# Optimization experiments

Hardware: AMD Instinct MI355X
Metric: run time of the kernel (lower is better)

## Reference

```python
import jax, jax.numpy as jnp
import numpy as np
import math


def _conv1x1(x, w, b):
    # x: [B,C,H,W], w: [O,C], b: [O] -> [B,O,H,W]
    return jnp.einsum('oc,bchw->bohw', w, x) + b[None, :, None, None]


def _attn_branch(x, f_w, f_b, g_w, g_b, h_w, h_b, gamma):
    B, C, H, W = x.shape
    N = H * W
    k_dim = C // 8
    f = _conv1x1(x, f_w, f_b).reshape(B, k_dim, N)  # [B,k,N]
    g = _conv1x1(x, g_w, g_b).reshape(B, k_dim, N)  # [B,k,N]
    # attention[b, n, m] = sum_k f[b,k,n] * g[b,k,m] / sqrt(k_dim)
    scores = jnp.einsum('bkn,bkm->bnm', f, g) / math.sqrt(k_dim)
    attn = jax.nn.softmax(scores, axis=2)  # softmax over last dim (dim=2)
    h = _conv1x1(x, h_w, h_b).reshape(B, C, N)  # [B,C,N]
    sa_map = jnp.einsum('bcn,bnm->bcm', h, attn).reshape(B, C, H, W)
    return gamma[0] * sa_map + x


def setup_inputs() -> dict:
    key = jax.random.key(0)
    ks = jax.random.split(key, 8)
    B, C, H, W = 4, 256, 64, 64
    kd = C // 8
    scale_in = 1.0 / math.sqrt(C)
    return {
        'x1': jax.random.normal(ks[0], (B, C, H, W), jnp.float32),
        'x2': jax.random.normal(ks[1], (B, C, H, W), jnp.float32),
        'f_w': jax.random.normal(ks[2], (kd, C), jnp.float32) * scale_in,
        'f_b': jnp.zeros((kd,), jnp.float32),
        'g_w': jax.random.normal(ks[3], (kd, C), jnp.float32) * scale_in,
        'g_b': jnp.zeros((kd,), jnp.float32),
        'h1_w': jax.random.normal(ks[4], (C, C), jnp.float32) * scale_in,
        'h1_b': jnp.zeros((C,), jnp.float32),
        'h2_w': jax.random.normal(ks[5], (C, C), jnp.float32) * scale_in,
        'h2_b': jnp.zeros((C,), jnp.float32),
        'gamma1': jax.random.normal(ks[6], (1,), jnp.float32),
        'gamma2': jax.random.normal(ks[7], (1,), jnp.float32),
    }


def reference(x1, x2, f_w, f_b, g_w, g_b, h1_w, h1_b, h2_w, h2_b, gamma1, gamma2):
    y1 = _attn_branch(x1, f_w, f_b, g_w, g_b, h1_w, h1_b, gamma1)
    y2 = _attn_branch(x2, f_w, f_b, g_w, g_b, h2_w, h2_b, gamma2)
    return (y1, y2)
```

## Files before the change

kernel.cpp:

```cpp
#include <hip/hip_runtime.h>
#include <hip/hip_bf16.h>
#include <math.h>

#define NDIM 4096
#define CDIM 256
#define KD   32
#define SCALE 0.17677669529663687f
#define SHIFT 8.0f

typedef __attribute__((ext_vector_type(8))) short short8;
typedef __attribute__((ext_vector_type(4))) float f32x4;
typedef unsigned short u16;
typedef unsigned int u32;

__device__ __forceinline__ u32 f2bf(float x) {
  union { float f; u32 u; } v; v.f = x;
  return (v.u + 0x7FFFu + ((v.u >> 16) & 1u)) >> 16;
}

__device__ __forceinline__ u32 pack_bf16x2(float a, float b) {
  __hip_bfloat162 h2 = __float22bfloat162_rn(make_float2(a, b));
  u32 r;
  __builtin_memcpy(&r, &h2, 4);
  return r;
}

#define MFMA16(a, b, c) __builtin_amdgcn_mfma_f32_16x16x32_bf16((a), (b), (c), 0, 0, 0)

__global__ void cast_all_kernel(const float* __restrict__ h1w,
                                const float* __restrict__ h2w,
                                const float* __restrict__ fw,
                                const float* __restrict__ gw,
                                u16* __restrict__ dst) {
  int i = blockIdx.x * 256 + threadIdx.x;
  float v;
  if (i < 65536) v = h1w[i];
  else if (i < 131072) v = h2w[i - 65536];
  else if (i < 139264) v = fw[i - 131072];
  else v = gw[i - 139264];
  dst[i] = (u16)f2bf(v);
}

__global__ __launch_bounds__(256) void transpose_cast_kernel(
    const float* __restrict__ x1, const float* __restrict__ x2,
    u16* __restrict__ xt) {
  __shared__ float ts[64][68];
  const int t = threadIdx.x;
  const int ntile = blockIdx.x * 64, Ctile = blockIdx.y * 64, z = blockIdx.z;
  const float* xb = ((z >> 2) ? x2 : x1) + (size_t)(z & 3) * CDIM * NDIM;
  u16* xtb = xt + (size_t)z * NDIM * CDIM;
  const int r = t >> 4, c4 = (t & 15) * 4;
#pragma unroll
  for (int i = 0; i < 4; i++) {
    float4 v = *(const float4*)&xb[(size_t)(Ctile + r + i * 16) * NDIM + ntile + c4];
    *(float4*)&ts[r + i * 16][c4] = v;
  }
  __syncthreads();
  const int n = t >> 2, Cg = (t & 3) * 16;
  u32 pk[8];
#pragma unroll
  for (int j = 0; j < 8; j++) {
    u32 lo = f2bf(ts[Cg + 2 * j][n]);
    u32 hi = f2bf(ts[Cg + 2 * j + 1][n]);
    pk[j] = lo | (hi << 16);
  }
  uint4* dst = (uint4*)&xtb[(size_t)(ntile + n) * CDIM + Ctile + Cg];
  dst[0] = make_uint4(pk[0], pk[1], pk[2], pk[3]);
  dst[1] = make_uint4(pk[4], pk[5], pk[6], pk[7]);
}

__global__ __launch_bounds__(256) void conv_fg_kernel(
    const u16* __restrict__ Wf, const float* __restrict__ fbias,
    const u16* __restrict__ Wg, const float* __restrict__ gbias,
    const u16* __restrict__ xt, u16* __restrict__ ftT, u16* __restrict__ gtT) {
  const int t = threadIdx.x, w = t >> 6, l = t & 63, li = l & 15, q = l >> 4;
  const int ntile = blockIdx.x * 64, bb = blockIdx.y;
  const u16* xtb = xt + (size_t)bb * NDIM * CDIM;
  f32x4 zero4 = {0.f, 0.f, 0.f, 0.f};
  f32x4 acc[2][2];
  for (int i = 0; i < 2; i++) for (int j = 0; j < 2; j++) acc[i][j] = zero4;
  const int nrow = ntile + w * 16 + li;

  for (int k0 = 0; k0 < CDIM; k0 += 32) {
    short8 bx = *(const short8*)&xtb[(size_t)nrow * CDIM + k0 + q * 8];
    short8 af0 = *(const short8*)&Wf[(size_t)(li) * CDIM + k0 + q * 8];
    short8 af1 = *(const short8*)&Wf[(size_t)(16 + li) * CDIM + k0 + q * 8];
    short8 ag0 = *(const short8*)&Wg[(size_t)(li) * CDIM + k0 + q * 8];
    short8 ag1 = *(const short8*)&Wg[(size_t)(16 + li) * CDIM + k0 + q * 8];
    acc[0][0] = MFMA16(af0, bx, acc[0][0]);
    acc[0][1] = MFMA16(af1, bx, acc[0][1]);
    acc[1][0] = MFMA16(ag0, bx, acc[1][0]);
    acc[1][1] = MFMA16(ag1, bx, acc[1][1]);
  }
  u16* outs[2] = {ftT + (size_t)bb * NDIM * KD, gtT + (size_t)bb * NDIM * KD};
  const float* biases[2] = {fbias, gbias};
#pragma unroll
  for (int fg = 0; fg < 2; fg++) {
#pragma unroll
    for (int os = 0; os < 2; os++) {
      float b0 = biases[fg][os * 16 + q * 4 + 0];
      float b1 = biases[fg][os * 16 + q * 4 + 1];
      float b2 = biases[fg][os * 16 + q * 4 + 2];
      float b3 = biases[fg][os * 16 + q * 4 + 3];
      u32 p0 = f2bf(acc[fg][os][0] + b0) | (f2bf(acc[fg][os][1] + b1) << 16);
      u32 p1 = f2bf(acc[fg][os][2] + b2) | (f2bf(acc[fg][os][3] + b3) << 16);
      *(uint2*)&outs[fg][(size_t)nrow * KD + os * 16 + q * 4] = make_uint2(p0, p1);
    }
  }
}

__global__ __launch_bounds__(256) void stats_kernel(
    const u16* __restrict__ ft, const u16* __restrict__ gt,
    float* __restrict__ L) {
  __shared__ float zred[32][64];
  const int t = threadIdx.x, w = t >> 6, l = t & 63, li = l & 15, q = l >> 4;
  const int n0 = blockIdx.x * 32;
  const int bb = blockIdx.z * 4 + blockIdx.y;
  const u16* ftb = ft + (size_t)bb * NDIM * KD;
  const u16* gtb = gt + (size_t)bb * NDIM * KD;
  f32x4 zero4 = {0.f, 0.f, 0.f, 0.f};

  short8 a0 = *(const short8*)&ftb[(size_t)(n0 + li) * KD + q * 8];
  short8 a1 = *(const short8*)&ftb[(size_t)(n0 + 16 + li) * KD + q * 8];
  f32x4 z0 = zero4, z1 = zero4;

#pragma unroll 2
  for (int it = 0; it < 64; it++) {
    int m = (it * 4 + w) * 16;
    short8 bf = *(const short8*)&gtb[(size_t)(m + li) * KD + q * 8];
    f32x4 S0 = MFMA16(a0, bf, zero4);
    f32x4 S1 = MFMA16(a1, bf, zero4);
#pragma unroll
    for (int reg = 0; reg < 4; reg++) {
      z0[reg] += __expf(S0[reg] * SCALE - SHIFT);
      z1[reg] += __expf(S1[reg] * SCALE - SHIFT);
    }
  }
#pragma unroll
  for (int reg = 0; reg < 4; reg++) {
    zred[q * 4 + reg][w * 16 + li] = z0[reg];
    zred[16 + q * 4 + reg][w * 16 + li] = z1[reg];
  }
  __syncthreads();
  const int r = t >> 3, i8 = t & 7;
  float4 s1 = *(const float4*)&zred[r][i8 * 8];
  float4 s2 = *(const float4*)&zred[r][i8 * 8 + 4];
  float sum = s1.x + s1.y + s1.z + s1.w + s2.x + s2.y + s2.z + s2.w;
  sum += __shfl_xor(sum, 1, 8);
  sum += __shfl_xor(sum, 2, 8);
  sum += __shfl_xor(sum, 4, 8);
  if (i8 == 0) L[(size_t)bb * NDIM + n0 + r] = SHIFT + __logf(sum);
}

__global__ __launch_bounds__(256) void conv_h_kernel(
    const u16* __restrict__ Wall, const float* __restrict__ b1,
    const float* __restrict__ b2, const u16* __restrict__ xt,
    const float* __restrict__ L, u16* __restrict__ outH) {
  const int t = threadIdx.x, w = t >> 6, l = t & 63, li = l & 15, q = l >> 4;
  const int ntile = blockIdx.x * 64;
  const int o0 = blockIdx.y * 64 + w * 16;
  const int bb = blockIdx.z, branch = bb >> 2;
  const u16* W = Wall + (size_t)branch * CDIM * CDIM;
  const float* bias = branch ? b2 : b1;
  const u16* xtb = xt + (size_t)bb * NDIM * CDIM;
  const float* Lb = L + (size_t)bb * NDIM;
  u16* ob = outH + (size_t)bb * CDIM * NDIM;
  f32x4 zero4 = {0.f, 0.f, 0.f, 0.f};
  f32x4 acc[4];
  for (int i = 0; i < 4; i++) acc[i] = zero4;

  for (int k0 = 0; k0 < CDIM; k0 += 32) {
    short8 a = *(const short8*)&W[(size_t)(o0 + li) * CDIM + k0 + q * 8];
#pragma unroll
    for (int ns = 0; ns < 4; ns++) {
      short8 bf = *(const short8*)&xtb[(size_t)(ntile + ns * 16 + li) * CDIM + k0 + q * 8];
      acc[ns] = MFMA16(a, bf, acc[ns]);
    }
  }
  float bv[4];
#pragma unroll
  for (int reg = 0; reg < 4; reg++) bv[reg] = bias[o0 + q * 4 + reg];
#pragma unroll
  for (int ns = 0; ns < 4; ns++) {
    int n = ntile + ns * 16 + li;
    float ex = __expf(-Lb[n]);
#pragma unroll
    for (int reg = 0; reg < 4; reg++) {
      int c = o0 + q * 4 + reg;
      ob[(size_t)c * NDIM + n] = (u16)f2bf((acc[ns][reg] + bv[reg]) * ex);
    }
  }
}

__global__ __launch_bounds__(1024, 4) void apply_kernel(
    const u16* __restrict__ ft, const u16* __restrict__ gt,
    const u16* __restrict__ h,
    const float* __restrict__ x1, const float* __restrict__ x2,
    const float* __restrict__ gamma1, const float* __restrict__ gamma2,
    float* __restrict__ out) {
  __shared__ u16 Pt[2][128][72];
  const int t = threadIdx.x, w = t >> 6, l = t & 63, li = l & 15, q = l >> 4;
  const int mtile = blockIdx.x * 128;
  const int b = blockIdx.y, br = blockIdx.z, bb = br * 4 + b;
  const u16* ftb = ft + (size_t)bb * NDIM * KD;
  const u16* gtb = gt + (size_t)bb * NDIM * KD;
  const u16* hb = h + (size_t)bb * CDIM * NDIM;
  const float* xb = (br ? x2 : x1) + (size_t)b * CDIM * NDIM;
  const float gmv = br ? gamma2[0] : gamma1[0];
  float* ob = out + (size_t)bb * CDIM * NDIM;

  const int msub_s = w >> 1, npair = w & 1;
  const int c0 = (w & 7) * 32;
  const int mg = (w >> 3) * 64;
  f32x4 zero4 = {0.f, 0.f, 0.f, 0.f};
  short8 gfrag = *(const short8*)&gtb[(size_t)(mtile + msub_s * 16 + li) * KD + q * 8];

  f32x4 acc[2][4];
  for (int i = 0; i < 2; i++) for (int j = 0; j < 4; j++) acc[i][j] = zero4;

  u32 Ppk[2][2];
  short8 afA[2];
#pragma unroll
  for (int j = 0; j < 2; j++) {
    int n = (npair * 2 + j) * 16;
    short8 a = *(const short8*)&ftb[(size_t)(n + li) * KD + q * 8];
    f32x4 S = MFMA16(a, gfrag, zero4);
    Ppk[j][0] = pack_bf16x2(__expf(S[0] * SCALE), __expf(S[1] * SCALE));
    Ppk[j][1] = pack_bf16x2(__expf(S[2] * SCALE), __expf(S[3] * SCALE));
  }
#pragma unroll
  for (int j = 0; j < 2; j++)
    afA[j] = *(const short8*)&ftb[(size_t)(64 + (npair * 2 + j) * 16 + li) * KD + q * 8];

  for (int i = 0; i < 64; i++) {
    const int n0 = i * 64;
    const int buf = i & 1;
    short8 ah[2][2];
#pragma unroll
    for (int cs = 0; cs < 2; cs++)
#pragma unroll
      for (int kh = 0; kh < 2; kh++)
        ah[cs][kh] = *(const short8*)
            &hb[(size_t)(c0 + cs * 16 + li) * NDIM + n0 + kh * 32 + q * 8];

#pragma unroll
    for (int j = 0; j < 2; j++)
      *(uint2*)&Pt[buf][msub_s * 16 + li][(npair * 2 + j) * 16 + q * 4] =
          make_uint2(Ppk[j][0], Ppk[j][1]);

#pragma unroll
    for (int j = 0; j < 2; j++) {
      f32x4 S = MFMA16(afA[j], gfrag, zero4);
      Ppk[j][0] = pack_bf16x2(__expf(S[0] * SCALE), __expf(S[1] * SCALE));
      Ppk[j][1] = pack_bf16x2(__expf(S[2] * SCALE), __expf(S[3] * SCALE));
    }

    __syncthreads();

    {
      int ch2 = (i + 2 < 64) ? i + 2 : 63;
#pragma unroll
      for (int j = 0; j < 2; j++) {
        int n = ch2 * 64 + (npair * 2 + j) * 16;
        afA[j] = *(const short8*)&ftb[(size_t)(n + li) * KD + q * 8];
      }
    }

#pragma unroll
    for (int kh = 0; kh < 2; kh++) {
#pragma unroll
      for (int ms = 0; ms < 4; ms++) {
        short8 bm = *(const short8*)&Pt[buf][mg + ms * 16 + li][kh * 32 + q * 8];
        acc[0][ms] = MFMA16(ah[0][kh], bm, acc[0][ms]);
        acc[1][ms] = MFMA16(ah[1][kh], bm, acc[1][ms]);
      }
    }
  }

#pragma unroll
  for (int cs = 0; cs < 2; cs++) {
#pragma unroll
    for (int ms = 0; ms < 4; ms++) {
#pragma unroll
      for (int reg = 0; reg < 4; reg++) {
        int c = c0 + cs * 16 + q * 4 + reg;
        int m = mtile + mg + ms * 16 + li;
        size_t idx = (size_t)c * NDIM + m;
        ob[idx] = gmv * acc[cs][ms][reg] + xb[idx];
      }
    }
  }
}

extern "C" void kernel_launch(void* const* d_in, const int* in_sizes, int n_in,
                              void* d_out, int out_size, void* d_ws, size_t ws_size,
                              hipStream_t stream) {
  const float* x1 = (const float*)d_in[0];
  const float* x2 = (const float*)d_in[1];
  const float* f_w = (const float*)d_in[2];
  const float* f_b = (const float*)d_in[3];
  const float* g_w = (const float*)d_in[4];
  const float* g_b = (const float*)d_in[5];
  const float* h1_w = (const float*)d_in[6];
  const float* h1_b = (const float*)d_in[7];
  const float* h2_w = (const float*)d_in[8];
  const float* h2_b = (const float*)d_in[9];
  const float* gamma1 = (const float*)d_in[10];
  const float* gamma2 = (const float*)d_in[11];
  float* out = (float*)d_out;

  char* ws = (char*)d_ws;
  u16* xt  = (u16*)(ws);
  u16* wh  = (u16*)(ws + 16777216);
  u16* ftw = (u16*)(ws + 33554432);
  u16* gtw = (u16*)(ws + 35651584);
  u16* wWh = (u16*)(ws + 37748736);
  u16* wWf = (u16*)(ws + 38010880);
  u16* wWg = (u16*)(ws + 38027264);
  float* Lw = (float*)(ws + 38043648);

  cast_all_kernel<<<576, 256, 0, stream>>>(h1_w, h2_w, f_w, g_w, wWh);

  transpose_cast_kernel<<<dim3(64, 4, 8), 256, 0, stream>>>(x1, x2, xt);

  conv_fg_kernel<<<dim3(64, 8), 256, 0, stream>>>(wWf, f_b, wWg, g_b, xt, ftw, gtw);

  stats_kernel<<<dim3(128, 4, 2), 256, 0, stream>>>(ftw, gtw, Lw);

  conv_h_kernel<<<dim3(64, 4, 8), 256, 0, stream>>>(wWh, h1_b, h2_b, xt, Lw, wh);

  apply_kernel<<<dim3(32, 4, 2), 1024, 0, stream>>>(ftw, gtw, wh, x1, x2,
                                                    gamma1, gamma2, out);
}
```

Baseline: 336.1 us.

## Halve apply kernel m-tile to 64 and double grid for more blocks

The apply kernel's m-tile shrinks from 128 to 64 columns, so the grid doubles to 512 blocks. Each wave now computes one score fragment per iteration instead of two and half as many output accumulators, with launch bounds raised to allow more resident blocks. The plain __syncthreads is replaced by an explicit LDS waitcnt plus raw barrier. The aim is better CU occupancy and load balance on a grid that was only 256 blocks. The cost is that every block re-reads the full h matrix for half the output, doubling h traffic relative to useful MFMA work.

Measured after the change: 440.7 us. 31.1% more time.

```diff
diff --git a/kernel.cpp b/kernel.cpp
--- a/kernel.cpp
+++ b/kernel.cpp
@@ -192,15 +192,15 @@
   }
 }
 
-__global__ __launch_bounds__(1024, 4) void apply_kernel(
+__global__ __launch_bounds__(1024, 8) void apply_kernel(
     const u16* __restrict__ ft, const u16* __restrict__ gt,
     const u16* __restrict__ h,
     const float* __restrict__ x1, const float* __restrict__ x2,
     const float* __restrict__ gamma1, const float* __restrict__ gamma2,
     float* __restrict__ out) {
-  __shared__ u16 Pt[2][128][72];
+  __shared__ u16 Pt[2][64][72];
   const int t = threadIdx.x, w = t >> 6, l = t & 63, li = l & 15, q = l >> 4;
-  const int mtile = blockIdx.x * 128;
+  const int mtile = blockIdx.x * 64;
   const int b = blockIdx.y, br = blockIdx.z, bb = br * 4 + b;
   const u16* ftb = ft + (size_t)bb * NDIM * KD;
   const u16* gtb = gt + (size_t)bb * NDIM * KD;
@@ -209,28 +209,25 @@
   const float gmv = br ? gamma2[0] : gamma1[0];
   float* ob = out + (size_t)bb * CDIM * NDIM;
 
-  const int msub_s = w >> 1, npair = w & 1;
+  const int msub_s = w & 3, ngrp = w >> 2;
   const int c0 = (w & 7) * 32;
-  const int mg = (w >> 3) * 64;
+  const int mg = (w >> 3) * 32;
   f32x4 zero4 = {0.f, 0.f, 0.f, 0.f};
   short8 gfrag = *(const short8*)&gtb[(size_t)(mtile + msub_s * 16 + li) * KD + q * 8];
 
-  f32x4 acc[2][4];
-  for (int i = 0; i < 2; i++) for (int j = 0; j < 4; j++) acc[i][j] = zero4;
-
-  u32 Ppk[2][2];
-  short8 afA[2];
-#pragma unroll
-  for (int j = 0; j < 2; j++) {
-    int n = (npair * 2 + j) * 16;
-    short8 a = *(const short8*)&ftb[(size_t)(n + li) * KD + q * 8];
+  f32x4 acc[2][2];
+  for (int i = 0; i < 2; i++) for (int j = 0; j < 2; j++) acc[i][j] = zero4;
+
+  u32 Ppk[2];
+  short8 afA;
+
+  {
+    short8 a = *(const short8*)&ftb[(size_t)(ngrp * 16 + li) * KD + q * 8];
     f32x4 S = MFMA16(a, gfrag, zero4);
-    Ppk[j][0] = pack_bf16x2(__expf(S[0] * SCALE), __expf(S[1] * SCALE));
-    Ppk[j][1] = pack_bf16x2(__expf(S[2] * SCALE), __expf(S[3] * SCALE));
-  }
-#pragma unroll
-  for (int j = 0; j < 2; j++)
-    afA[j] = *(const short8*)&ftb[(size_t)(64 + (npair * 2 + j) * 16 + li) * KD + q * 8];
+    Ppk[0] = pack_bf16x2(__expf(S[0] * SCALE), __expf(S[1] * SCALE));
+    Ppk[1] = pack_bf16x2(__expf(S[2] * SCALE), __expf(S[3] * SCALE));
+  }
+  afA = *(const short8*)&ftb[(size_t)(64 + ngrp * 16 + li) * KD + q * 8];
 
   for (int i = 0; i < 64; i++) {
     const int n0 = i * 64;
@@ -243,33 +240,27 @@
         ah[cs][kh] = *(const short8*)
             &hb[(size_t)(c0 + cs * 16 + li) * NDIM + n0 + kh * 32 + q * 8];
 
-#pragma unroll
-    for (int j = 0; j < 2; j++)
-      *(uint2*)&Pt[buf][msub_s * 16 + li][(npair * 2 + j) * 16 + q * 4] =
-          make_uint2(Ppk[j][0], Ppk[j][1]);
-
-#pragma unroll
-    for (int j = 0; j < 2; j++) {
-      f32x4 S = MFMA16(afA[j], gfrag, zero4);
-      Ppk[j][0] = pack_bf16x2(__expf(S[0] * SCALE), __expf(S[1] * SCALE));
-      Ppk[j][1] = pack_bf16x2(__expf(S[2] * SCALE), __expf(S[3] * SCALE));
-    }
-
-    __syncthreads();
+    *(uint2*)&Pt[buf][msub_s * 16 + li][ngrp * 16 + q * 4] =
+        make_uint2(Ppk[0], Ppk[1]);
+
+    {
+      f32x4 S = MFMA16(afA, gfrag, zero4);
+      Ppk[0] = pack_bf16x2(__expf(S[0] * SCALE), __expf(S[1] * SCALE));
+      Ppk[1] = pack_bf16x2(__expf(S[2] * SCALE), __expf(S[3] * SCALE));
+    }
+
+    asm volatile("s_waitcnt lgkmcnt(0)" ::: "memory");
+    __builtin_amdgcn_s_barrier();
 
     {
       int ch2 = (i + 2 < 64) ? i + 2 : 63;
-#pragma unroll
-      for (int j = 0; j < 2; j++) {
-        int n = ch2 * 64 + (npair * 2 + j) * 16;
-        afA[j] = *(const short8*)&ftb[(size_t)(n + li) * KD + q * 8];
-      }
+      afA = *(const short8*)&ftb[(size_t)(ch2 * 64 + ngrp * 16 + li) * KD + q * 8];
     }
 
 #pragma unroll
     for (int kh = 0; kh < 2; kh++) {
 #pragma unroll
-      for (int ms = 0; ms < 4; ms++) {
+      for (int ms = 0; ms < 2; ms++) {
         short8 bm = *(const short8*)&Pt[buf][mg + ms * 16 + li][kh * 32 + q * 8];
         acc[0][ms] = MFMA16(ah[0][kh], bm, acc[0][ms]);
         acc[1][ms] = MFMA16(ah[1][kh], bm, acc[1][ms]);
@@ -280,7 +271,7 @@
 #pragma unroll
   for (int cs = 0; cs < 2; cs++) {
 #pragma unroll
-    for (int ms = 0; ms < 4; ms++) {
+    for (int ms = 0; ms < 2; ms++) {
 #pragma unroll
       for (int reg = 0; reg < 4; reg++) {
         int c = c0 + cs * 16 + q * 4 + reg;
@@ -329,6 +320,6 @@
 
   conv_h_kernel<<<dim3(64, 4, 8), 256, 0, stream>>>(wWh, h1_b, h2_b, xt, Lw, wh);
 
-  apply_kernel<<<dim3(32, 4, 2), 1024, 0, stream>>>(ftw, gtw, wh, x1, x2,
+  apply_kernel<<<dim3(64, 4, 2), 1024, 0, stream>>>(ftw, gtw, wh, x1, x2,
                                                     gamma1, gamma2, out);
 }
```
